# Performance work log

Measured on AMD Instinct MI355X. Metric: run time of the kernel, lower is better.

The kernel has to match this reference:

```python
import jax, jax.numpy as jnp
import numpy as np

B, S, D = 1, 1024, 4096
NH, NKV, HD = 32, 8, 128
CACHE = 1024


def setup_inputs() -> dict:
    key = jax.random.key(0)
    ks = jax.random.split(key, 9)
    return {
        "hidden_states": jax.random.normal(ks[0], (B, S, D), jnp.float32),
        "freqs_cos": jax.random.uniform(ks[1], (S, HD // 2), jnp.float32),
        "freqs_sin": jax.random.uniform(ks[2], (S, HD // 2), jnp.float32),
        "atten_mask": jnp.zeros((S, CACHE + S), jnp.float32),
        "k_cache": jax.random.normal(ks[3], (B, NKV, HD, CACHE), jnp.float32),
        "v_cache": jax.random.normal(ks[4], (B, NKV, CACHE, HD), jnp.float32),
        "wq": jax.random.normal(ks[5], (NH, HD, D), jnp.float32) * 0.02,
        "wk": jax.random.normal(ks[6], (NKV, HD, D), jnp.float32) * 0.02,
        "wv": jax.random.normal(ks[7], (NKV, HD, D), jnp.float32) * 0.02,
        "wo": jax.random.normal(ks[8], (D, NH * HD), jnp.float32) * 0.02,
    }


def _rope(x, cos, sin):
    # x: [b, s, h, hd]; cos/sin: [s, hd//2]
    half = x.shape[-1] // 2
    xr, xi = x[..., :half], x[..., half:]
    c = cos[None, :, None, :]
    sn = sin[None, :, None, :]
    return jnp.concatenate([xr * c - xi * sn, xr * sn + xi * c], axis=-1)


def reference(hidden_states, freqs_cos, freqs_sin, atten_mask, k_cache, v_cache, wq, wk, wv, wo):
    b, s, d = hidden_states.shape
    nh, hd, _ = wq.shape
    nkv = wk.shape[0]
    g = nh // nkv  # query heads per KV head
    scale = float(hd) ** 0.5

    # projections (equivalent to per-head 1x1 convs)
    q = jnp.einsum("bsd,hed->bshe", hidden_states, wq)   # [b,s,nh,hd]
    k = jnp.einsum("bsd,hed->bshe", hidden_states, wk)   # [b,s,nkv,hd]
    v = jnp.einsum("bsd,hed->bshe", hidden_states, wv)   # [b,s,nkv,hd]

    q = _rope(q, freqs_cos, freqs_sin)
    k = _rope(k, freqs_cos, freqs_sin)

    # concat KV cache: kh [b,nkv,hd,KV], vh [b,nkv,KV,hd]
    kh = jnp.concatenate([k_cache, k.transpose(0, 2, 3, 1)], axis=-1)
    vh = jnp.concatenate([v_cache, v.transpose(0, 2, 1, 3)], axis=2)

    # grouped attention: head i uses kv group i // g
    qg = q.reshape(b, s, nkv, g, hd).transpose(0, 2, 3, 1, 4)  # [b,n,g,s,e]
    scores = jnp.einsum("bngse,bnet->bngst", qg, kh) / scale + atten_mask
    p = jax.nn.softmax(scores, axis=-1)
    yg = jnp.einsum("bngst,bnte->bngse", p, vh)               # [b,n,g,s,e]
    y = yg.transpose(0, 3, 1, 2, 4).reshape(b, s, nh * hd)     # head order n*g+j

    y = jnp.einsum("bsf,df->bsd", y, wo)
    return (y, kh, vh)
```

## Files before the change

### kernel.cpp

```cpp
#include <hip/hip_runtime.h>
#include <hip/hip_bf16.h>
#include <stdint.h>

#define S_LEN 1024
#define D_MODEL 4096
#define NHEAD 32
#define NKV 8
#define HD 128
#define CACHE_T 1024
#define T_TOT 2048
#define NQKV 6144

typedef __attribute__((ext_vector_type(8))) short short8;
typedef __attribute__((ext_vector_type(4))) float floatx4;

__device__ __forceinline__ unsigned short f2bf(float f) {
  union { float f; uint32_t u; } v; v.f = f;
  uint32_t r = v.u + 0x7FFFu + ((v.u >> 16) & 1u);
  return (unsigned short)(r >> 16);
}

__device__ __forceinline__ void gload_lds16(const void* g, void* s) {
  __builtin_amdgcn_global_load_lds((const __attribute__((address_space(1))) void*)g,
                                   (__attribute__((address_space(3))) void*)s, 16, 0, 0);
}

__global__ void convf2b_kernel(const float* __restrict__ in, unsigned short* __restrict__ out, int n8) {
  int stride = gridDim.x * blockDim.x;
  for (int t = blockIdx.x * blockDim.x + threadIdx.x; t < n8; t += stride) {
    int i = t * 8;
    floatx4 a = *(const floatx4*)(in + i);
    floatx4 b = *(const floatx4*)(in + i + 4);
    short8 o;
    o[0] = (short)f2bf(a[0]); o[1] = (short)f2bf(a[1]); o[2] = (short)f2bf(a[2]); o[3] = (short)f2bf(a[3]);
    o[4] = (short)f2bf(b[0]); o[5] = (short)f2bf(b[1]); o[6] = (short)f2bf(b[2]); o[7] = (short)f2bf(b[3]);
    *(short8*)(out + i) = o;
  }
}

__global__ void mask_flag_kernel(const float* __restrict__ m, int n, int* __restrict__ flag) {
  int stride = gridDim.x * blockDim.x;
  bool nz = false;
  for (int i = blockIdx.x * blockDim.x + threadIdx.x; i < n; i += stride)
    nz |= (m[i] != 0.0f);
  if (nz) atomicOr(flag, 1);
}

__global__ __launch_bounds__(256, 3)
void gemm_bf_kernel(const unsigned short* __restrict__ A,
                    const unsigned short* __restrict__ W,
                    float* __restrict__ C,
                    int M, int N, int K, int ldc, int GM)
{
  __shared__ __align__(16) unsigned char As[2][64 * 128];
  __shared__ __align__(16) unsigned char Bs[2][128 * 128];

  const int nwg = gridDim.x;
  int orig = blockIdx.x;
  int wg = (orig & 7) * (nwg >> 3) + (orig >> 3);
  const int mt = wg % GM, nt = wg / GM;
  const int m0 = mt * 64, n0 = nt * 128;

  const int tid = threadIdx.x;
  const int wid = tid >> 6, lane = tid & 63;
  const int g4 = lane >> 4, r16 = lane & 15;
  const int wr = (wid >> 1) * 32, wc = (wid & 1) * 64;

  const int lr = lane >> 3, lc = lane & 7;
  const unsigned short* Arow[2];
  const unsigned short* Wrow[4];
#pragma unroll
  for (int i = 0; i < 2; ++i) {
    int r = (wid * 2 + i) * 8 + lr;
    Arow[i] = A + (size_t)(m0 + r) * K + (lc ^ (r & 7)) * 8;
  }
#pragma unroll
  for (int i = 0; i < 4; ++i) {
    int r = (wid * 4 + i) * 8 + lr;
    Wrow[i] = W + (size_t)(n0 + r) * K + (lc ^ (r & 7)) * 8;
  }

  auto stage = [&](int buf, int kt) {
    const int kb = kt * 64;
#pragma unroll
    for (int i = 0; i < 2; ++i)
      gload_lds16(Arow[i] + kb, &As[buf][(wid * 2 + i) * 1024]);
#pragma unroll
    for (int i = 0; i < 4; ++i)
      gload_lds16(Wrow[i] + kb, &Bs[buf][(wid * 4 + i) * 1024]);
  };

  floatx4 acc[2][4];
#pragma unroll
  for (int m = 0; m < 2; ++m)
#pragma unroll
    for (int n = 0; n < 4; ++n) acc[m][n] = (floatx4){0.f, 0.f, 0.f, 0.f};

  const int NK = K >> 6;
  stage(0, 0);
  __syncthreads();
  int cur = 0;
  for (int kt = 0; kt < NK; ++kt) {
    if (kt + 1 < NK) stage(cur ^ 1, kt + 1);
#pragma unroll
    for (int kk = 0; kk < 2; ++kk) {
      const int kb = kk * 64 + g4 * 16;
      short8 af[2], bf[4];
#pragma unroll
      for (int m = 0; m < 2; ++m) {
        int row = wr + m * 16 + r16;
        af[m] = *(const short8*)(&As[cur][row * 128 + (kb ^ ((row & 7) << 4))]);
      }
#pragma unroll
      for (int n = 0; n < 4; ++n) {
        int row = wc + n * 16 + r16;
        bf[n] = *(const short8*)(&Bs[cur][row * 128 + (kb ^ ((row & 7) << 4))]);
      }
#pragma unroll
      for (int m = 0; m < 2; ++m)
#pragma unroll
        for (int n = 0; n < 4; ++n)
          acc[m][n] = __builtin_amdgcn_mfma_f32_16x16x32_bf16(af[m], bf[n], acc[m][n], 0, 0, 0);
    }
    __syncthreads();
    cur ^= 1;
  }

#pragma unroll
  for (int m = 0; m < 2; ++m)
#pragma unroll
    for (int n = 0; n < 4; ++n)
#pragma unroll
      for (int j = 0; j < 4; ++j)
        C[(size_t)(m0 + wr + m * 16 + g4 * 4 + j) * ldc + (n0 + wc + n * 16 + r16)] = acc[m][n][j];
}

__global__ __launch_bounds__(256, 2)
void gemm_kernel(const unsigned short* __restrict__ A,
                 const float* __restrict__ W0, const float* __restrict__ W1, const float* __restrict__ W2,
                 int n1, int n2,
                 float* __restrict__ C,
                 int M, int N, int K, int GM)
{
  __shared__ __align__(16) unsigned char As[2][128 * 128];
  __shared__ __align__(16) unsigned char Bs[2][128 * 128];

  const int nwg = gridDim.x;
  int orig = blockIdx.x;
  int xcd = orig & 7, loc = orig >> 3;
  int q = nwg >> 3, r = nwg & 7;
  int wg = (xcd < r ? xcd * (q + 1) : r * (q + 1) + (xcd - r) * q) + loc;
  const int mt = wg % GM, nt = wg / GM;
  const int m0 = mt * 128, n0 = nt * 128;

  const int tid = threadIdx.x;
  const int wid = tid >> 6, lane = tid & 63;
  const int g4 = lane >> 4, r16 = lane & 15;
  const int wr = (wid >> 1) * 64, wc = (wid & 1) * 64;

  int srow[4], skc[4];
  const float* wptr[4];
#pragma unroll
  for (int i = 0; i < 4; ++i) {
    int c = tid + 256 * i;
    srow[i] = c >> 3; skc[i] = c & 7;
    int ng = n0 + srow[i];
    wptr[i] = (ng < n1) ? (W0 + (size_t)ng * K)
            : (ng < n2) ? (W1 + (size_t)(ng - n1) * K)
                        : (W2 + (size_t)(ng - n2) * K);
  }

  short8 ar[4]; floatx4 br[8];
  auto load_tile = [&](int kt) {
    int kb = kt * 64;
#pragma unroll
    for (int i = 0; i < 4; ++i) {
      ar[i] = *(const short8*)(A + (size_t)(m0 + srow[i]) * K + kb + skc[i] * 8);
      br[2 * i]     = *(const floatx4*)(wptr[i] + kb + skc[i] * 8);
      br[2 * i + 1] = *(const floatx4*)(wptr[i] + kb + skc[i] * 8 + 4);
    }
  };
  auto write_tile = [&](int buf) {
#pragma unroll
    for (int i = 0; i < 4; ++i) {
      int off = srow[i] * 128 + ((skc[i] * 16) ^ ((srow[i] & 7) << 4));
      *(short8*)(&As[buf][off]) = ar[i];
      short8 bb;
      bb[0] = (short)f2bf(br[2 * i][0]);     bb[1] = (short)f2bf(br[2 * i][1]);
      bb[2] = (short)f2bf(br[2 * i][2]);     bb[3] = (short)f2bf(br[2 * i][3]);
      bb[4] = (short)f2bf(br[2 * i + 1][0]); bb[5] = (short)f2bf(br[2 * i + 1][1]);
      bb[6] = (short)f2bf(br[2 * i + 1][2]); bb[7] = (short)f2bf(br[2 * i + 1][3]);
      *(short8*)(&Bs[buf][off]) = bb;
    }
  };

  floatx4 acc[4][4];
#pragma unroll
  for (int m = 0; m < 4; ++m)
#pragma unroll
    for (int n = 0; n < 4; ++n) acc[m][n] = (floatx4){0.f, 0.f, 0.f, 0.f};

  const int NK = K >> 6;
  load_tile(0);
  write_tile(0);
  __syncthreads();
  int cur = 0;
  for (int kt = 0; kt < NK; ++kt) {
    if (kt + 1 < NK) load_tile(kt + 1);
#pragma unroll
    for (int kk = 0; kk < 2; ++kk) {
      const int kb = kk * 32 + g4 * 8;
      short8 af[4], bfr[4];
#pragma unroll
      for (int m = 0; m < 4; ++m) {
        int row = wr + m * 16 + r16;
        af[m] = *(const short8*)(&As[cur][row * 128 + ((kb * 2) ^ ((row & 7) << 4))]);
      }
#pragma unroll
      for (int n = 0; n < 4; ++n) {
        int row = wc + n * 16 + r16;
        bfr[n] = *(const short8*)(&Bs[cur][row * 128 + ((kb * 2) ^ ((row & 7) << 4))]);
      }
#pragma unroll
      for (int m = 0; m < 4; ++m)
#pragma unroll
        for (int n = 0; n < 4; ++n)
          acc[m][n] = __builtin_amdgcn_mfma_f32_16x16x32_bf16(af[m], bfr[n], acc[m][n], 0, 0, 0);
    }
    if (kt + 1 < NK) write_tile(cur ^ 1);
    __syncthreads();
    cur ^= 1;
  }

#pragma unroll
  for (int m = 0; m < 4; ++m)
#pragma unroll
    for (int n = 0; n < 4; ++n)
#pragma unroll
      for (int j = 0; j < 4; ++j)
        C[(size_t)(m0 + wr + m * 16 + g4 * 4 + j) * N + (n0 + wc + n * 16 + r16)] = acc[m][n][j];
}

__global__ void rope_q_kernel(const float* __restrict__ qkv, const float* __restrict__ fc,
                              const float* __restrict__ fs, unsigned short* __restrict__ qb)
{
  const int s = blockIdx.x, t = threadIdx.x;
  const int head = t >> 3, e0 = (t & 7) * 8;
  const float* base = qkv + (size_t)s * NQKV + head * HD + e0;
  floatx4 xr0 = *(const floatx4*)(base);
  floatx4 xr1 = *(const floatx4*)(base + 4);
  floatx4 xi0 = *(const floatx4*)(base + 64);
  floatx4 xi1 = *(const floatx4*)(base + 68);
  floatx4 c0 = *(const floatx4*)(fc + s * 64 + e0);
  floatx4 c1 = *(const floatx4*)(fc + s * 64 + e0 + 4);
  floatx4 s0 = *(const floatx4*)(fs + s * 64 + e0);
  floatx4 s1 = *(const floatx4*)(fs + s * 64 + e0 + 4);
  short8 outr, outi;
#pragma unroll
  for (int j = 0; j < 4; ++j) {
    outr[j]     = (short)f2bf(xr0[j] * c0[j] - xi0[j] * s0[j]);
    outr[4 + j] = (short)f2bf(xr1[j] * c1[j] - xi1[j] * s1[j]);
    outi[j]     = (short)f2bf(xr0[j] * s0[j] + xi0[j] * c0[j]);
    outi[4 + j] = (short)f2bf(xr1[j] * s1[j] + xi1[j] * c1[j]);
  }
  unsigned short* ob = qb + (size_t)s * D_MODEL + head * HD + e0;
  *(short8*)ob = outr;
  *(short8*)(ob + 64) = outi;
}

__global__ void rope_k_kernel(const float* __restrict__ qkv, const float* __restrict__ fc,
                              const float* __restrict__ fs, float* __restrict__ kh,
                              unsigned short* __restrict__ khb)
{
  __shared__ float T[128][65];
  const int n = blockIdx.x >> 4, s0 = (blockIdx.x & 15) * 64;
  const int tid = threadIdx.x;
  const int sl = tid >> 2, e0 = (tid & 3) * 16;
  const int s = s0 + sl;
  const float* base = qkv + (size_t)s * NQKV + D_MODEL + n * HD;
  float xr[16], xi[16], cc[16], sn[16];
#pragma unroll
  for (int i = 0; i < 16; i += 4) {
    *(floatx4*)(xr + i) = *(const floatx4*)(base + e0 + i);
    *(floatx4*)(xi + i) = *(const floatx4*)(base + 64 + e0 + i);
    *(floatx4*)(cc + i) = *(const floatx4*)(fc + s * 64 + e0 + i);
    *(floatx4*)(sn + i) = *(const floatx4*)(fs + s * 64 + e0 + i);
  }
  short8 r0, r1, i0, i1;
#pragma unroll
  for (int i = 0; i < 16; ++i) {
    float vr = xr[i] * cc[i] - xi[i] * sn[i];
    float vi = xr[i] * sn[i] + xi[i] * cc[i];
    T[e0 + i][sl] = vr;
    T[64 + e0 + i][sl] = vi;
    unsigned short br = f2bf(vr), bi = f2bf(vi);
    if (i < 8) { r0[i] = (short)br; i0[i] = (short)bi; }
    else       { r1[i - 8] = (short)br; i1[i - 8] = (short)bi; }
  }
  unsigned short* kb = khb + ((size_t)n * T_TOT + CACHE_T + s) * HD;
  *(short8*)(kb + e0) = r0;       *(short8*)(kb + e0 + 8) = r1;
  *(short8*)(kb + 64 + e0) = i0;  *(short8*)(kb + 64 + e0 + 8) = i1;
  __syncthreads();
  const int e = tid >> 1, hf = tid & 1;
  float* dst = kh + ((size_t)n * HD + e) * T_TOT + CACHE_T + s0 + hf * 32;
#pragma unroll
  for (int i = 0; i < 32; i += 4) {
    floatx4 v;
    v[0] = T[e][hf * 32 + i]; v[1] = T[e][hf * 32 + i + 1];
    v[2] = T[e][hf * 32 + i + 2]; v[3] = T[e][hf * 32 + i + 3];
    *(floatx4*)(dst + i) = v;
  }
}

__global__ void v_scatter_kernel(const float* __restrict__ qkv, float* __restrict__ vh,
                                 unsigned short* __restrict__ vtb)
{
  __shared__ __align__(16) unsigned short T[128][72];
  const int n = blockIdx.x >> 4, s0 = (blockIdx.x & 15) * 64;
  const int tid = threadIdx.x;
  const int sl = tid >> 2, e0 = (tid & 3) * 32;
  const float* src = qkv + (size_t)(s0 + sl) * NQKV + D_MODEL + NKV * HD + n * HD + e0;
  float* dst = vh + ((size_t)n * T_TOT + CACHE_T + s0 + sl) * HD + e0;
#pragma unroll
  for (int i = 0; i < 32; i += 4) {
    floatx4 v = *(const floatx4*)(src + i);
    *(floatx4*)(dst + i) = v;
    T[e0 + i][sl] = f2bf(v[0]); T[e0 + i + 1][sl] = f2bf(v[1]);
    T[e0 + i + 2][sl] = f2bf(v[2]); T[e0 + i + 3][sl] = f2bf(v[3]);
  }
  __syncthreads();
  const int e = tid >> 1, hf = tid & 1;
  unsigned short* ob = vtb + ((size_t)n * HD + e) * T_TOT + CACHE_T + s0 + hf * 32;
#pragma unroll
  for (int i = 0; i < 32; i += 8) *(short8*)(ob + i) = *(const short8*)(&T[e][hf * 32 + i]);
}

__global__ void cache_k_kernel(const float* __restrict__ kc, float* __restrict__ kh,
                               unsigned short* __restrict__ khb)
{
  __shared__ __align__(16) unsigned short T[64][72];
  const int b = blockIdx.x;
  const int n = b >> 5, et = (b >> 4) & 1, tt = b & 15;
  const int e0 = et * 64, t0 = tt * 64;
  const int tid = threadIdx.x;
  const int el = tid >> 2, tc = (tid & 3) * 16;
  const float* src = kc + ((size_t)n * HD + e0 + el) * CACHE_T + t0 + tc;
  float* dst = kh + ((size_t)n * HD + e0 + el) * T_TOT + t0 + tc;
#pragma unroll
  for (int i = 0; i < 16; i += 4) {
    floatx4 v = *(const floatx4*)(src + i);
    *(floatx4*)(dst + i) = v;
    T[tc + i][el] = f2bf(v[0]); T[tc + i + 1][el] = f2bf(v[1]);
    T[tc + i + 2][el] = f2bf(v[2]); T[tc + i + 3][el] = f2bf(v[3]);
  }
  __syncthreads();
  const int tl = tid >> 2, ec = (tid & 3) * 16;
  unsigned short* ob = khb + ((size_t)n * T_TOT + t0 + tl) * HD + e0 + ec;
#pragma unroll
  for (int i = 0; i < 16; i += 8) *(short8*)(ob + i) = *(const short8*)(&T[tl][ec + i]);
}

__global__ void cache_v_kernel(const float* __restrict__ vc, float* __restrict__ vh,
                               unsigned short* __restrict__ vtb)
{
  __shared__ __align__(16) unsigned short T[128][72];
  const int n = blockIdx.x >> 4, t0 = (blockIdx.x & 15) * 64;
  const int tid = threadIdx.x;
  const int tl = tid >> 2, e0 = (tid & 3) * 32;
  const float* src = vc + ((size_t)n * CACHE_T + t0 + tl) * HD + e0;
  float* dst = vh + ((size_t)n * T_TOT + t0 + tl) * HD + e0;
#pragma unroll
  for (int i = 0; i < 32; i += 4) {
    floatx4 v = *(const floatx4*)(src + i);
    *(floatx4*)(dst + i) = v;
    T[e0 + i][tl] = f2bf(v[0]); T[e0 + i + 1][tl] = f2bf(v[1]);
    T[e0 + i + 2][tl] = f2bf(v[2]); T[e0 + i + 3][tl] = f2bf(v[3]);
  }
  __syncthreads();
  const int e = tid >> 1, hf = tid & 1;
  unsigned short* ob = vtb + ((size_t)n * HD + e) * T_TOT + t0 + hf * 32;
#pragma unroll
  for (int i = 0; i < 32; i += 8) *(short8*)(ob + i) = *(const short8*)(&T[e][hf * 32 + i]);
}

__global__ __launch_bounds__(256, 2)
void attn_kernel(const unsigned short* __restrict__ Qb, const unsigned short* __restrict__ Kb,
                 const unsigned short* __restrict__ Vb, const float* __restrict__ mask,
                 const int* __restrict__ flag, unsigned short* __restrict__ Ob)
{
  __shared__ __align__(16) unsigned char KL[2][64 * 256];
  __shared__ __align__(16) unsigned char VL[2][128 * 128];
  __shared__ __align__(16) unsigned short PL[4][16][64];

  int orig = blockIdx.x;
  int wg = (orig & 7) * 64 + (orig >> 3);
  const int nkv = wg >> 6;
  const int inner = wg & 63;
  const int h = nkv * 4 + (inner >> 4);
  const int qt = inner & 15;

  const int tid = threadIdx.x, wid = tid >> 6, lane = tid & 63;
  const int g4 = lane >> 4, r16 = lane & 15;
  const int srow = qt * 64 + wid * 16;
  const bool use_mask = (*flag) != 0;

  short8 qf[4];
#pragma unroll
  for (int ks = 0; ks < 4; ++ks)
    qf[ks] = *(const short8*)(Qb + (size_t)(srow + r16) * D_MODEL + h * HD + ks * 32 + g4 * 8);

  floatx4 acc[8];
#pragma unroll
  for (int fe = 0; fe < 8; ++fe) acc[fe] = (floatx4){0.f, 0.f, 0.f, 0.f};
  float mrow[4] = {-1e30f, -1e30f, -1e30f, -1e30f};
  float lrow[4] = {0.f, 0.f, 0.f, 0.f};

  const unsigned short* Kbase = Kb + (size_t)nkv * T_TOT * HD;
  const unsigned short* Vbase = Vb + (size_t)nkv * HD * T_TOT;
  const float sscale = 0.08838834764831845f;

  const unsigned short* kp[4];
  const unsigned short* vp[4];
  int kbase_off[4], vbase_off[4];
#pragma unroll
  for (int i = 0; i < 4; ++i) {
    int krow = wid * 16 + i * 4 + (lane >> 4);
    int kch  = (lane & 15) ^ (krow & 7);
    kp[i] = Kbase + (size_t)krow * HD + kch * 8;
    kbase_off[i] = (wid * 16 + i * 4) * 256;
    int vrow = wid * 32 + i * 8 + (lane >> 3);
    int vch  = (lane & 7) ^ (vrow & 7);
    vp[i] = Vbase + (size_t)vrow * T_TOT + vch * 8;
    vbase_off[i] = (wid * 32 + i * 8) * 128;
  }

#pragma unroll
  for (int i = 0; i < 4; ++i) gload_lds16(kp[i], &KL[0][kbase_off[i]]);
#pragma unroll
  for (int i = 0; i < 4; ++i) gload_lds16(vp[i], &VL[0][vbase_off[i]]);
#pragma unroll
  for (int i = 0; i < 4; ++i) { kp[i] += 64 * HD; vp[i] += 64; }
  __syncthreads();

  int cur = 0;
  for (int t0 = 0; t0 < T_TOT; t0 += 64) {
    if (t0 + 64 < T_TOT) {
#pragma unroll
      for (int i = 0; i < 4; ++i) gload_lds16(kp[i], &KL[cur ^ 1][kbase_off[i]]);
#pragma unroll
      for (int i = 0; i < 4; ++i) gload_lds16(vp[i], &VL[cur ^ 1][vbase_off[i]]);
#pragma unroll
      for (int i = 0; i < 4; ++i) { kp[i] += 64 * HD; vp[i] += 64; }
    }

    floatx4 sc[4];
#pragma unroll
    for (int fc4 = 0; fc4 < 4; ++fc4) {
      sc[fc4] = (floatx4){0.f, 0.f, 0.f, 0.f};
      const int trow = fc4 * 16 + r16;
#pragma unroll
      for (int ks = 0; ks < 4; ++ks) {
        short8 kf = *(const short8*)(&KL[cur][trow * 256 + (((ks * 32 + g4 * 8) * 2) ^ ((trow & 7) << 4))]);
        sc[fc4] = __builtin_amdgcn_mfma_f32_16x16x32_bf16(qf[ks], kf, sc[fc4], 0, 0, 0);
      }
    }

    float sv[4][4];
#pragma unroll
    for (int fc4 = 0; fc4 < 4; ++fc4)
#pragma unroll
      for (int j = 0; j < 4; ++j) {
        float x = sc[fc4][j] * sscale;
        if (use_mask) x += mask[(size_t)(srow + g4 * 4 + j) * T_TOT + t0 + fc4 * 16 + r16];
        sv[fc4][j] = x;
      }

#pragma unroll
    for (int j = 0; j < 4; ++j) {
      float mx = fmaxf(fmaxf(sv[0][j], sv[1][j]), fmaxf(sv[2][j], sv[3][j]));
      mx = fmaxf(mx, __shfl_xor(mx, 1));
      mx = fmaxf(mx, __shfl_xor(mx, 2));
      mx = fmaxf(mx, __shfl_xor(mx, 4));
      mx = fmaxf(mx, __shfl_xor(mx, 8));
      float mn = fmaxf(mrow[j], mx);
      float corr = __expf(mrow[j] - mn);
      mrow[j] = mn;
      float ss = 0.f;
#pragma unroll
      for (int fc4 = 0; fc4 < 4; ++fc4) {
        float p = __expf(sv[fc4][j] - mn);
        sv[fc4][j] = p;
        ss += p;
      }
      ss += __shfl_xor(ss, 1); ss += __shfl_xor(ss, 2);
      ss += __shfl_xor(ss, 4); ss += __shfl_xor(ss, 8);
      lrow[j] = lrow[j] * corr + ss;
#pragma unroll
      for (int fe = 0; fe < 8; ++fe) acc[fe][j] *= corr;
    }

#pragma unroll
    for (int fc4 = 0; fc4 < 4; ++fc4)
#pragma unroll
      for (int j = 0; j < 4; ++j) {
        const int prow = g4 * 4 + j;
        PL[wid][prow][(fc4 * 16 + r16) ^ ((prow & 7) << 3)] = f2bf(sv[fc4][j]);
      }

    short8 pf[2];
#pragma unroll
    for (int ks = 0; ks < 2; ++ks)
      pf[ks] = *(const short8*)(&PL[wid][r16][(ks * 32 + g4 * 8) ^ ((r16 & 7) << 3)]);
#pragma unroll
    for (int fe = 0; fe < 8; ++fe) {
      const int erow = fe * 16 + r16;
#pragma unroll
      for (int ks = 0; ks < 2; ++ks) {
        short8 vf = *(const short8*)(&VL[cur][erow * 128 + (((ks * 32 + g4 * 8) * 2) ^ ((erow & 7) << 4))]);
        acc[fe] = __builtin_amdgcn_mfma_f32_16x16x32_bf16(pf[ks], vf, acc[fe], 0, 0, 0);
      }
    }
    __syncthreads();
    cur ^= 1;
  }

#pragma unroll
  for (int j = 0; j < 4; ++j) {
    float inv = 1.0f / lrow[j];
    const size_t rowb = (size_t)(srow + g4 * 4 + j) * D_MODEL + h * HD;
#pragma unroll
    for (int fe = 0; fe < 8; ++fe)
      Ob[rowb + fe * 16 + r16] = f2bf(acc[fe][j] * inv);
  }
}

extern "C" void kernel_launch(void* const* d_in, const int* in_sizes, int n_in,
                              void* d_out, int out_size, void* d_ws, size_t ws_size,
                              hipStream_t stream)
{
  const float* hs   = (const float*)d_in[0];
  const float* fc   = (const float*)d_in[1];
  const float* fs   = (const float*)d_in[2];
  const float* mask = (const float*)d_in[3];
  const float* kc   = (const float*)d_in[4];
  const float* vc   = (const float*)d_in[5];
  const float* wq   = (const float*)d_in[6];
  const float* wk   = (const float*)d_in[7];
  const float* wv   = (const float*)d_in[8];
  const float* wo   = (const float*)d_in[9];

  float* y  = (float*)d_out;
  float* kh = y + (size_t)S_LEN * D_MODEL;
  float* vh = kh + (size_t)NKV * HD * T_TOT;

  char* ws = (char*)d_ws;
  unsigned short* hs_b   = (unsigned short*)ws;
  float* qkv             = (float*)(ws + 8388608u);
  unsigned short* attn_o = (unsigned short*)(ws + 8388608u);
  unsigned short* khb    = (unsigned short*)(ws + 33554432u);
  unsigned short* vtb    = (unsigned short*)(ws + 37748736u);
  int* flag              = (int*)(ws + 41943040u);
  unsigned short* slotW  = (unsigned short*)(ws + 41943296u);

  const size_t base = 41943296ull;
  const bool big = ws_size >= base + 50331648ull;
  const bool mid = ws_size >= base + 33554432ull;

  hipMemsetAsync(flag, 0, 4, stream);
  mask_flag_kernel<<<256, 256, 0, stream>>>(mask, S_LEN * T_TOT, flag);
  convf2b_kernel<<<2048, 256, 0, stream>>>(hs, hs_b, S_LEN * D_MODEL / 8);

  if (big) {
    convf2b_kernel<<<2048, 256, 0, stream>>>(wq, slotW, NHEAD * HD * D_MODEL / 8);
    convf2b_kernel<<<2048, 256, 0, stream>>>(wk, slotW + (size_t)4096 * 4096, NKV * HD * D_MODEL / 8);
    convf2b_kernel<<<2048, 256, 0, stream>>>(wv, slotW + (size_t)5120 * 4096, NKV * HD * D_MODEL / 8);
    gemm_bf_kernel<<<768, 256, 0, stream>>>(hs_b, slotW, qkv, 1024, 6144, 4096, 6144, 16);
  } else if (mid) {
    convf2b_kernel<<<2048, 256, 0, stream>>>(wk, slotW, NKV * HD * D_MODEL / 8);
    convf2b_kernel<<<2048, 256, 0, stream>>>(wv, slotW + (size_t)1024 * 4096, NKV * HD * D_MODEL / 8);
    gemm_bf_kernel<<<256, 256, 0, stream>>>(hs_b, slotW, qkv + 4096, 1024, 2048, 4096, 6144, 16);
    convf2b_kernel<<<2048, 256, 0, stream>>>(wq, slotW, NHEAD * HD * D_MODEL / 8);
    gemm_bf_kernel<<<512, 256, 0, stream>>>(hs_b, slotW, qkv, 1024, 4096, 4096, 6144, 16);
  } else {
    gemm_kernel<<<384, 256, 0, stream>>>(hs_b, wq, wk, wv, 4096, 5120, qkv, 1024, 6144, 4096, 8);
  }

  rope_q_kernel<<<1024, 256, 0, stream>>>(qkv, fc, fs, hs_b);
  rope_k_kernel<<<128, 256, 0, stream>>>(qkv, fc, fs, kh, khb);
  v_scatter_kernel<<<128, 256, 0, stream>>>(qkv, vh, vtb);
  cache_k_kernel<<<256, 256, 0, stream>>>(kc, kh, khb);
  cache_v_kernel<<<128, 256, 0, stream>>>(vc, vh, vtb);
  attn_kernel<<<512, 256, 0, stream>>>(hs_b, khb, vtb, mask, flag, attn_o);

  if (mid) {
    convf2b_kernel<<<2048, 256, 0, stream>>>(wo, slotW, D_MODEL * D_MODEL / 8);
    gemm_bf_kernel<<<512, 256, 0, stream>>>(attn_o, slotW, y, 1024, 4096, 4096, 4096, 16);
  } else {
    gemm_kernel<<<256, 256, 0, stream>>>(attn_o, wo, wo, wo, 1 << 29, 1 << 29, y, 1024, 4096, 4096, 8);
  }
}
```

Baseline: 287.6 us.

## Split attention KV range across workgroups with combine kernel, fold scale into Q

Attention is split-KV: the grid doubles and each workgroup handles half the keys. It writes unnormalized partial outputs and per-row max and sum to workspace, and a new combine kernel merges the two halves into bf16. The softmax scale moves into the RoPE-Q kernel. The LDS double buffer becomes a single buffer so launch bounds can target 4 blocks per CU, and the rescale is skipped when no row max grows. In exchange it loses load/compute overlap within a workgroup, adds extra fp32 partial traffic plus one more launch, and needs a larger workspace (otherwise it falls back to no split).

```diff
diff --git a/kernel.cpp b/kernel.cpp
--- a/kernel.cpp
+++ b/kernel.cpp
@@ -10,6 +10,7 @@
 #define CACHE_T 1024
 #define T_TOT 2048
 #define NQKV 6144
+#define QSCALE 0.08838834764831845f
 
 typedef __attribute__((ext_vector_type(8))) short short8;
 typedef __attribute__((ext_vector_type(4))) float floatx4;
@@ -258,10 +259,10 @@
   short8 outr, outi;
 #pragma unroll
   for (int j = 0; j < 4; ++j) {
-    outr[j]     = (short)f2bf(xr0[j] * c0[j] - xi0[j] * s0[j]);
-    outr[4 + j] = (short)f2bf(xr1[j] * c1[j] - xi1[j] * s1[j]);
-    outi[j]     = (short)f2bf(xr0[j] * s0[j] + xi0[j] * c0[j]);
-    outi[4 + j] = (short)f2bf(xr1[j] * s1[j] + xi1[j] * c1[j]);
+    outr[j]     = (short)f2bf((xr0[j] * c0[j] - xi0[j] * s0[j]) * QSCALE);
+    outr[4 + j] = (short)f2bf((xr1[j] * c1[j] - xi1[j] * s1[j]) * QSCALE);
+    outi[j]     = (short)f2bf((xr0[j] * s0[j] + xi0[j] * c0[j]) * QSCALE);
+    outi[4 + j] = (short)f2bf((xr1[j] * s1[j] + xi1[j] * c1[j]) * QSCALE);
   }
   unsigned short* ob = qb + (size_t)s * D_MODEL + head * HD + e0;
   *(short8*)ob = outr;
@@ -383,21 +384,27 @@
   for (int i = 0; i < 32; i += 8) *(short8*)(ob + i) = *(const short8*)(&T[e][hf * 32 + i]);
 }
 
-__global__ __launch_bounds__(256, 2)
+__global__ __launch_bounds__(256, 4)
 void attn_kernel(const unsigned short* __restrict__ Qb, const unsigned short* __restrict__ Kb,
                  const unsigned short* __restrict__ Vb, const float* __restrict__ mask,
-                 const int* __restrict__ flag, unsigned short* __restrict__ Ob)
-{
-  __shared__ __align__(16) unsigned char KL[2][64 * 256];
-  __shared__ __align__(16) unsigned char VL[2][128 * 128];
+                 const int* __restrict__ flag, unsigned short* __restrict__ Ob,
+                 float* __restrict__ Upart, float* __restrict__ mlpart, int nsplit)
+{
+  __shared__ __align__(16) unsigned char KL[64 * 256];
+  __shared__ __align__(16) unsigned char VL[128 * 128];
   __shared__ __align__(16) unsigned short PL[4][16][64];
 
+  const int nwg = gridDim.x;
   int orig = blockIdx.x;
-  int wg = (orig & 7) * 64 + (orig >> 3);
-  const int nkv = wg >> 6;
-  const int inner = wg & 63;
+  int wg = (orig & 7) * (nwg >> 3) + (orig >> 3);
+  const int bpn = nwg >> 3;
+  const int nkv = wg / bpn;
+  const int rem = wg - nkv * bpn;
+  const int kvs = rem >> 6;
+  const int inner = rem & 63;
   const int h = nkv * 4 + (inner >> 4);
   const int qt = inner & 15;
+  const int TKV = T_TOT / nsplit;
 
   const int tid = threadIdx.x, wid = tid >> 6, lane = tid & 63;
   const int g4 = lane >> 4, r16 = lane & 15;
@@ -415,9 +422,8 @@
   float mrow[4] = {-1e30f, -1e30f, -1e30f, -1e30f};
   float lrow[4] = {0.f, 0.f, 0.f, 0.f};
 
-  const unsigned short* Kbase = Kb + (size_t)nkv * T_TOT * HD;
-  const unsigned short* Vbase = Vb + (size_t)nkv * HD * T_TOT;
-  const float sscale = 0.08838834764831845f;
+  const unsigned short* Kbase = Kb + (size_t)nkv * T_TOT * HD + (size_t)kvs * TKV * HD;
+  const unsigned short* Vbase = Vb + (size_t)nkv * HD * T_TOT + (size_t)kvs * TKV;
 
   const unsigned short* kp[4];
   const unsigned short* vp[4];
@@ -434,24 +440,14 @@
     vbase_off[i] = (wid * 32 + i * 8) * 128;
   }
 
-#pragma unroll
-  for (int i = 0; i < 4; ++i) gload_lds16(kp[i], &KL[0][kbase_off[i]]);
-#pragma unroll
-  for (int i = 0; i < 4; ++i) gload_lds16(vp[i], &VL[0][vbase_off[i]]);
-#pragma unroll
-  for (int i = 0; i < 4; ++i) { kp[i] += 64 * HD; vp[i] += 64; }
-  __syncthreads();
-
-  int cur = 0;
-  for (int t0 = 0; t0 < T_TOT; t0 += 64) {
-    if (t0 + 64 < T_TOT) {
-#pragma unroll
-      for (int i = 0; i < 4; ++i) gload_lds16(kp[i], &KL[cur ^ 1][kbase_off[i]]);
-#pragma unroll
-      for (int i = 0; i < 4; ++i) gload_lds16(vp[i], &VL[cur ^ 1][vbase_off[i]]);
-#pragma unroll
-      for (int i = 0; i < 4; ++i) { kp[i] += 64 * HD; vp[i] += 64; }
-    }
+  for (int t0 = 0; t0 < TKV; t0 += 64) {
+#pragma unroll
+    for (int i = 0; i < 4; ++i) gload_lds16(kp[i], &KL[kbase_off[i]]);
+#pragma unroll
+    for (int i = 0; i < 4; ++i) gload_lds16(vp[i], &VL[vbase_off[i]]);
+#pragma unroll
+    for (int i = 0; i < 4; ++i) { kp[i] += 64 * HD; vp[i] += 64; }
+    __syncthreads();
 
     floatx4 sc[4];
 #pragma unroll
@@ -460,7 +456,7 @@
       const int trow = fc4 * 16 + r16;
 #pragma unroll
       for (int ks = 0; ks < 4; ++ks) {
-        short8 kf = *(const short8*)(&KL[cur][trow * 256 + (((ks * 32 + g4 * 8) * 2) ^ ((trow & 7) << 4))]);
+        short8 kf = *(const short8*)(&KL[trow * 256 + (((ks * 32 + g4 * 8) * 2) ^ ((trow & 7) << 4))]);
         sc[fc4] = __builtin_amdgcn_mfma_f32_16x16x32_bf16(qf[ks], kf, sc[fc4], 0, 0, 0);
       }
     }
@@ -470,33 +466,46 @@
     for (int fc4 = 0; fc4 < 4; ++fc4)
 #pragma unroll
       for (int j = 0; j < 4; ++j) {
-        float x = sc[fc4][j] * sscale;
-        if (use_mask) x += mask[(size_t)(srow + g4 * 4 + j) * T_TOT + t0 + fc4 * 16 + r16];
+        float x = sc[fc4][j];
+        if (use_mask) x += mask[(size_t)(srow + g4 * 4 + j) * T_TOT + kvs * TKV + t0 + fc4 * 16 + r16];
         sv[fc4][j] = x;
       }
 
+    float mx[4];
+    bool up = false;
 #pragma unroll
     for (int j = 0; j < 4; ++j) {
-      float mx = fmaxf(fmaxf(sv[0][j], sv[1][j]), fmaxf(sv[2][j], sv[3][j]));
-      mx = fmaxf(mx, __shfl_xor(mx, 1));
-      mx = fmaxf(mx, __shfl_xor(mx, 2));
-      mx = fmaxf(mx, __shfl_xor(mx, 4));
-      mx = fmaxf(mx, __shfl_xor(mx, 8));
-      float mn = fmaxf(mrow[j], mx);
-      float corr = __expf(mrow[j] - mn);
-      mrow[j] = mn;
+      float m0 = fmaxf(fmaxf(sv[0][j], sv[1][j]), fmaxf(sv[2][j], sv[3][j]));
+      m0 = fmaxf(m0, __shfl_xor(m0, 1));
+      m0 = fmaxf(m0, __shfl_xor(m0, 2));
+      m0 = fmaxf(m0, __shfl_xor(m0, 4));
+      m0 = fmaxf(m0, __shfl_xor(m0, 8));
+      mx[j] = m0;
+      up = up || (m0 > mrow[j]);
+    }
+    if (__any(up)) {
+#pragma unroll
+      for (int j = 0; j < 4; ++j) {
+        float mn = fmaxf(mrow[j], mx[j]);
+        float corr = __expf(mrow[j] - mn);
+        mrow[j] = mn;
+        lrow[j] *= corr;
+#pragma unroll
+        for (int fe = 0; fe < 8; ++fe) acc[fe][j] *= corr;
+      }
+    }
+#pragma unroll
+    for (int j = 0; j < 4; ++j) {
       float ss = 0.f;
 #pragma unroll
       for (int fc4 = 0; fc4 < 4; ++fc4) {
-        float p = __expf(sv[fc4][j] - mn);
+        float p = __expf(sv[fc4][j] - mrow[j]);
         sv[fc4][j] = p;
         ss += p;
       }
       ss += __shfl_xor(ss, 1); ss += __shfl_xor(ss, 2);
       ss += __shfl_xor(ss, 4); ss += __shfl_xor(ss, 8);
-      lrow[j] = lrow[j] * corr + ss;
-#pragma unroll
-      for (int fe = 0; fe < 8; ++fe) acc[fe][j] *= corr;
+      lrow[j] += ss;
     }
 
 #pragma unroll
@@ -516,22 +525,61 @@
       const int erow = fe * 16 + r16;
 #pragma unroll
       for (int ks = 0; ks < 2; ++ks) {
-        short8 vf = *(const short8*)(&VL[cur][erow * 128 + (((ks * 32 + g4 * 8) * 2) ^ ((erow & 7) << 4))]);
+        short8 vf = *(const short8*)(&VL[erow * 128 + (((ks * 32 + g4 * 8) * 2) ^ ((erow & 7) << 4))]);
         acc[fe] = __builtin_amdgcn_mfma_f32_16x16x32_bf16(pf[ks], vf, acc[fe], 0, 0, 0);
       }
     }
     __syncthreads();
-    cur ^= 1;
-  }
-
-#pragma unroll
-  for (int j = 0; j < 4; ++j) {
-    float inv = 1.0f / lrow[j];
-    const size_t rowb = (size_t)(srow + g4 * 4 + j) * D_MODEL + h * HD;
-#pragma unroll
-    for (int fe = 0; fe < 8; ++fe)
-      Ob[rowb + fe * 16 + r16] = f2bf(acc[fe][j] * inv);
-  }
+  }
+
+  if (nsplit == 2) {
+#pragma unroll
+    for (int j = 0; j < 4; ++j) {
+      const size_t R = (size_t)h * S_LEN + srow + g4 * 4 + j;
+      float* Ur = Upart + ((size_t)kvs * (NHEAD * S_LEN) + R) * HD;
+#pragma unroll
+      for (int fe = 0; fe < 8; ++fe) Ur[fe * 16 + r16] = acc[fe][j];
+      if (r16 == 0) {
+        float* mlp = mlpart + ((size_t)kvs * (NHEAD * S_LEN) + R) * 2;
+        mlp[0] = mrow[j]; mlp[1] = lrow[j];
+      }
+    }
+  } else {
+#pragma unroll
+    for (int j = 0; j < 4; ++j) {
+      float inv = 1.0f / lrow[j];
+      const size_t rowb = (size_t)(srow + g4 * 4 + j) * D_MODEL + h * HD;
+#pragma unroll
+      for (int fe = 0; fe < 8; ++fe)
+        Ob[rowb + fe * 16 + r16] = f2bf(acc[fe][j] * inv);
+    }
+  }
+}
+
+__global__ void attn_combine_kernel(const float* __restrict__ U, const float* __restrict__ ml,
+                                    unsigned short* __restrict__ Ob)
+{
+  const int t = blockIdx.x * 256 + threadIdx.x;
+  const int r = t >> 4;
+  const int e0 = (t & 15) * 8;
+  const float m1 = ml[(size_t)r * 2],                  l1 = ml[(size_t)r * 2 + 1];
+  const float m2 = ml[((size_t)(NHEAD * S_LEN) + r) * 2], l2 = ml[((size_t)(NHEAD * S_LEN) + r) * 2 + 1];
+  const float M = fmaxf(m1, m2);
+  const float a1 = __expf(m1 - M), a2 = __expf(m2 - M);
+  const float inv = 1.0f / (l1 * a1 + l2 * a2);
+  const float* u1 = U + (size_t)r * HD + e0;
+  const float* u2 = U + (size_t)(NHEAD * S_LEN) * HD + (size_t)r * HD + e0;
+  floatx4 x1a = *(const floatx4*)u1, x1b = *(const floatx4*)(u1 + 4);
+  floatx4 x2a = *(const floatx4*)u2, x2b = *(const floatx4*)(u2 + 4);
+  const int s = r & (S_LEN - 1), hh = r >> 10;
+  unsigned short* ob = Ob + (size_t)s * D_MODEL + hh * HD + e0;
+  short8 o;
+#pragma unroll
+  for (int k = 0; k < 4; ++k) {
+    o[k]     = (short)f2bf((x1a[k] * a1 + x2a[k] * a2) * inv);
+    o[4 + k] = (short)f2bf((x1b[k] * a1 + x2b[k] * a2) * inv);
+  }
+  *(short8*)ob = o;
 }
 
 extern "C" void kernel_launch(void* const* d_in, const int* in_sizes, int n_in,
@@ -565,6 +613,9 @@
   const size_t base = 41943296ull;
   const bool big = ws_size >= base + 50331648ull;
   const bool mid = ws_size >= base + 33554432ull;
+  const int nsplit = (ws_size >= base + 34078720ull) ? 2 : 1;
+  float* Upart  = (float*)(ws + base);
+  float* mlpart = (float*)(ws + base + 33554432u);
 
   hipMemsetAsync(flag, 0, 4, stream);
   mask_flag_kernel<<<256, 256, 0, stream>>>(mask, S_LEN * T_TOT, flag);
@@ -590,7 +641,11 @@
   v_scatter_kernel<<<128, 256, 0, stream>>>(qkv, vh, vtb);
   cache_k_kernel<<<256, 256, 0, stream>>>(kc, kh, khb);
   cache_v_kernel<<<128, 256, 0, stream>>>(vc, vh, vtb);
-  attn_kernel<<<512, 256, 0, stream>>>(hs_b, khb, vtb, mask, flag, attn_o);
+
+  attn_kernel<<<512 * nsplit, 256, 0, stream>>>(hs_b, khb, vtb, mask, flag, attn_o,
+                                                Upart, mlpart, nsplit);
+  if (nsplit == 2)
+    attn_combine_kernel<<<2048, 256, 0, stream>>>(Upart, mlpart, attn_o);
 
   if (mid) {
     convf2b_kernel<<<2048, 256, 0, stream>>>(wo, slotW, D_MODEL * D_MODEL / 8);
```

After: 304.5 us. +5.9%, slower.
